# Kernel optimization log

Hardware: AMD Instinct MI355X
Metric: run time of the kernel (lower is better)

## Reference

```python
import jax, jax.numpy as jnp
import numpy as np

EMB = 1024

def setup_inputs() -> dict:
    key = jax.random.key(0)
    ks = jax.random.split(key, 6)
    T, k1, k2, D = 64, 256, 1024, EMB
    scale = 1.0 / np.sqrt(D)
    return {
        "fast_feature": jax.random.normal(ks[0], (T, k2, D), jnp.float32),
        "slow_feature": jax.random.normal(ks[1], (T, k1, D), jnp.float32),
        "fast_W": jax.random.normal(ks[2], (D, D), jnp.float32) * scale,
        "fast_b": jax.random.normal(ks[3], (D,), jnp.float32) * 0.01,
        "slow_W": jax.random.normal(ks[4], (D, D), jnp.float32) * scale,
        "slow_b": jax.random.normal(ks[5], (D,), jnp.float32) * 0.01,
    }

def reference(fast_feature, slow_feature, fast_W, fast_b, slow_W, slow_b):
    # Linear projections (torch Linear: x @ W.T + b)
    fast_key = jnp.einsum('tkd,ed->tke', fast_feature, fast_W) + fast_b  # [T,k2,D]
    slow_key = jnp.einsum('tkd,ed->tke', slow_feature, slow_W) + slow_b  # [T,k1,D]
    # Scaled dot-product similarity fast->slow
    sim = jnp.einsum('tqd,tkd->tqk', fast_key, slow_key)  # [T,k2,k1]
    sim = sim / jnp.sqrt(jnp.asarray(slow_feature.shape[-1], sim.dtype))
    attn = jax.nn.softmax(sim, axis=-1)
    ctx = jnp.einsum('tqk,tkd->tqd', attn, slow_feature)  # note: values are raw slow_feature
    return fast_feature + ctx
```

## Files before the change

kernel.cpp:

```cpp
#include <hip/hip_runtime.h>
#include <stdint.h>

typedef __attribute__((ext_vector_type(8))) short bf16x8;
typedef __attribute__((ext_vector_type(4))) float f32x4;

__device__ __forceinline__ unsigned short f2bf(float f) {
  unsigned int u = __builtin_bit_cast(unsigned int, f);
  u += 0x7FFFu + ((u >> 16) & 1u);
  return (unsigned short)(u >> 16);
}

__device__ __forceinline__ void gload_lds16(const void* g, void* l) {
  __builtin_amdgcn_global_load_lds(
      (__attribute__((address_space(1))) void*)(uintptr_t)g,
      (__attribute__((address_space(3))) void*)l,
      16, 0, 0);
}

#define BARRIER() do { asm volatile("" ::: "memory"); __builtin_amdgcn_s_barrier(); asm volatile("" ::: "memory"); } while (0)
#define WAITVM(N) asm volatile("s_waitcnt vmcnt(" #N ")" ::: "memory")

template <int MODE>
__global__ __launch_bounds__(512, 2) void gemm8(
    const unsigned short* __restrict__ A, const unsigned short* __restrict__ B,
    void* __restrict__ Cv, const float* __restrict__ aux, int N, int K,
    int nm, int nn, long sAB, long sBB, long sCB, long sXB, float scale)
{
  __shared__ __align__(16) char lds[131072];
  char* ldsc = lds;

  const int tid = threadIdx.x;
  const int lane = tid & 63;
  const int wid = tid >> 6;
  const int fr = lane & 15, fq = lane >> 4;

  const int nwg = gridDim.x;
  const int id = blockIdx.x;
  const int swz = (id & 7) * (nwg >> 3) + (id >> 3);
  const int per = nm * nn;
  const int t = swz / per;
  const int rem = swz - t * per;
  const int mi_ = rem / nn, ni_ = rem - mi_ * nn;
  const long bm = (long)mi_ * 256, bn = (long)ni_ * 256;

  const unsigned short* Ag = A + (long)t * sAB + bm * K;
  const unsigned short* Bg = B + (long)t * sBB + bn * K;
  const int NT = K >> 6;

  const unsigned short* aS[2][2];
  const unsigned short* bS[2][2];
#pragma unroll
  for (int p = 0; p < 2; ++p) {
    const int q = p * 512 + tid;
    const int lr = q >> 3, cs = q & 7;
    const int cl = cs ^ (lr & 7);
#pragma unroll
    for (int h = 0; h < 2; ++h) {
      const int gA = ((lr >> 6) << 7) | (h << 6) | (lr & 63);
      const int gB = ((lr >> 5) << 6) | (h << 5) | (lr & 31);
      aS[p][h] = Ag + (long)gA * K + cl * 8;
      bS[p][h] = Bg + (long)gB * K + cl * 8;
    }
  }

  const int c0 = ((fq ^ (fr & 3)) + ((fr >> 2) & 1) * 4) * 16;
  const int aRd = ((wid >> 2) * 64 + fr) * 128 + c0;
  const int bRd = ((wid & 3) * 32 + fr) * 128 + c0;

  f32x4 acc[2][2][4][2];
#pragma unroll
  for (int a = 0; a < 2; a++)
#pragma unroll
    for (int b = 0; b < 2; b++)
#pragma unroll
      for (int i = 0; i < 4; i++)
#pragma unroll
        for (int j = 0; j < 2; j++)
#pragma unroll
          for (int r = 0; r < 4; r++) acc[a][b][i][j][r] = 0.f;

  bf16x8 af[4][2], bf[2][2][2];

#define STAGE(srcArr, aoff, h, ktv, b) do {                                   \
  _Pragma("unroll")                                                           \
  for (int p = 0; p < 2; ++p)                                                 \
    gload_lds16(srcArr[p][h] + ((long)(ktv) << 6),                            \
                ldsc + (aoff) + ((b) << 16) + ((h) << 14) + (p << 13) + (wid << 10)); \
} while (0)

#define LDA(mi, cub) do {                                                     \
  _Pragma("unroll")                                                           \
  for (int i = 0; i < 4; ++i) {                                               \
    af[i][0] = *(const bf16x8*)(ldsc + (cub) + (mi) * 16384 + aRd + i * 2048);        \
    af[i][1] = *(const bf16x8*)(ldsc + (cub) + (mi) * 16384 + (aRd ^ 64) + i * 2048); \
  }                                                                           \
} while (0)

#define LDB(nj, cub) do {                                                     \
  _Pragma("unroll")                                                           \
  for (int j = 0; j < 2; ++j) {                                               \
    bf[nj][j][0] = *(const bf16x8*)(ldsc + 32768 + (cub) + (nj) * 16384 + bRd + j * 2048);        \
    bf[nj][j][1] = *(const bf16x8*)(ldsc + 32768 + (cub) + (nj) * 16384 + (bRd ^ 64) + j * 2048); \
  }                                                                           \
} while (0)

#define QUAD(mi, nj) do {                                                     \
  __builtin_amdgcn_s_setprio(1);                                              \
  _Pragma("unroll")                                                           \
  for (int i = 0; i < 4; ++i)                                                 \
  _Pragma("unroll")                                                           \
  for (int j = 0; j < 2; ++j) {                                               \
    acc[mi][nj][i][j] = __builtin_amdgcn_mfma_f32_16x16x32_bf16(              \
        af[i][0], bf[nj][j][0], acc[mi][nj][i][j], 0, 0, 0);                  \
    acc[mi][nj][i][j] = __builtin_amdgcn_mfma_f32_16x16x32_bf16(              \
        af[i][1], bf[nj][j][1], acc[mi][nj][i][j], 0, 0, 0);                  \
  }                                                                           \
  __builtin_amdgcn_s_setprio(0);                                              \
} while (0)

  STAGE(aS, 0, 0, 0, 0);
  STAGE(bS, 32768, 0, 0, 0);
  STAGE(bS, 32768, 1, 0, 0);
  STAGE(aS, 0, 1, 0, 0);
  if (NT > 1) {
    STAGE(aS, 0, 0, 1, 1);
    STAGE(bS, 32768, 0, 1, 1);
    STAGE(bS, 32768, 1, 1, 1);
    WAITVM(6);
  } else {
    WAITVM(0);
  }
  BARRIER();

  for (int kt = 0; kt < NT; ++kt) {
    const int cur = kt & 1, nxt = cur ^ 1;
    const int cub = cur << 16;
    LDA(0, cub);
    LDB(0, cub);
    if (kt + 1 < NT) STAGE(aS, 0, 1, kt + 1, nxt);
    BARRIER();
    QUAD(0, 0);
    BARRIER();
    LDB(1, cub);
    if (kt + 2 < NT) STAGE(aS, 0, 0, kt + 2, cur);
    BARRIER();
    QUAD(0, 1);
    BARRIER();
    LDA(1, cub);
    if (kt + 2 < NT) STAGE(bS, 32768, 0, kt + 2, cur);
    BARRIER();
    QUAD(1, 0);
    BARRIER();
    if (kt + 2 < NT) {
      STAGE(bS, 32768, 1, kt + 2, cur);
      QUAD(1, 1);
      WAITVM(6);
    } else {
      QUAD(1, 1);
      WAITVM(0);
    }
    BARRIER();
  }

  if (MODE == 1) {
    float* red  = (float*)ldsc;
    float* red2 = (float*)(ldsc + 4096);
    const int wc = wid & 3;
    const int rbase = (wid >> 2) * 128;
#pragma unroll
    for (int mi = 0; mi < 2; ++mi)
#pragma unroll
      for (int i = 0; i < 4; ++i)
#pragma unroll
        for (int r = 0; r < 4; ++r) {
          float m = fmaxf(fmaxf(acc[mi][0][i][0][r], acc[mi][0][i][1][r]),
                          fmaxf(acc[mi][1][i][0][r], acc[mi][1][i][1][r]));
#pragma unroll
          for (int o = 1; o <= 8; o <<= 1) m = fmaxf(m, __shfl_xor(m, o));
          if (fr == 0) red[(rbase + mi * 64 + i * 16 + fq * 4 + r) * 4 + wc] = m;
        }
    BARRIER();
#pragma unroll
    for (int mi = 0; mi < 2; ++mi)
#pragma unroll
      for (int i = 0; i < 4; ++i)
#pragma unroll
        for (int r = 0; r < 4; ++r) {
          const int rl = rbase + mi * 64 + i * 16 + fq * 4 + r;
          f32x4 mm = *(f32x4*)&red[rl * 4];
          const float M = fmaxf(fmaxf(mm[0], mm[1]), fmaxf(mm[2], mm[3]));
          float s = 0.f;
#pragma unroll
          for (int nj = 0; nj < 2; ++nj)
#pragma unroll
            for (int j = 0; j < 2; ++j) {
              float e = __expf((acc[mi][nj][i][j][r] - M) * scale);
              acc[mi][nj][i][j][r] = e;
              s += e;
            }
#pragma unroll
          for (int o = 1; o <= 8; o <<= 1) s += __shfl_xor(s, o);
          if (fr == 0) red2[rl * 4 + wc] = s;
        }
    BARRIER();
    unsigned short* C = (unsigned short*)Cv + (long)t * sCB;
#pragma unroll
    for (int mi = 0; mi < 2; ++mi)
#pragma unroll
      for (int i = 0; i < 4; ++i)
#pragma unroll
        for (int r = 0; r < 4; ++r) {
          const int rl = rbase + mi * 64 + i * 16 + fq * 4 + r;
          f32x4 sv = *(f32x4*)&red2[rl * 4];
          const float inv = 1.0f / (sv[0] + sv[1] + sv[2] + sv[3]);
          const long gr = bm + rl;
#pragma unroll
          for (int nj = 0; nj < 2; ++nj)
#pragma unroll
            for (int j = 0; j < 2; ++j) {
              const long gcol = bn + wc * 64 + nj * 32 + j * 16 + fr;
              C[gr * N + gcol] = f2bf(acc[mi][nj][i][j][r] * inv);
            }
        }
  } else {
#pragma unroll
    for (int mi = 0; mi < 2; ++mi)
#pragma unroll
      for (int nj = 0; nj < 2; ++nj)
#pragma unroll
        for (int i = 0; i < 4; ++i) {
          const long grow0 = bm + (wid >> 2) * 128 + mi * 64 + i * 16 + fq * 4;
#pragma unroll
          for (int j = 0; j < 2; ++j) {
            const long gcol = bn + (wid & 3) * 64 + nj * 32 + j * 16 + fr;
            if (MODE == 0) {
              unsigned short* C = (unsigned short*)Cv + (long)t * sCB;
              const float bv = aux[gcol];
#pragma unroll
              for (int r = 0; r < 4; ++r)
                C[(grow0 + r) * N + gcol] = f2bf(acc[mi][nj][i][j][r] + bv);
            } else {
              float* C = (float*)Cv + (long)t * sCB;
              const float* X = aux + (long)t * sXB;
#pragma unroll
              for (int r = 0; r < 4; ++r) {
                const long idx = (grow0 + r) * N + gcol;
                C[idx] = acc[mi][nj][i][j][r] + X[idx];
              }
            }
          }
        }
  }
#undef STAGE
#undef LDA
#undef LDB
#undef QUAD
}

__global__ __launch_bounds__(256) void convert_f32_bf16(
    const float* __restrict__ in, unsigned short* __restrict__ out, long n) {
  long i = ((long)blockIdx.x * 256 + threadIdx.x) * 4;
  long stride = (long)gridDim.x * 1024;
  for (; i < n; i += stride) {
    float4 v = *(const float4*)(in + i);
    ushort4 o;
    o.x = f2bf(v.x); o.y = f2bf(v.y); o.z = f2bf(v.z); o.w = f2bf(v.w);
    *(ushort4*)(out + i) = o;
  }
}

__global__ __launch_bounds__(256) void convert_transpose_slow(
    const float* __restrict__ in, unsigned short* __restrict__ outR,
    unsigned short* __restrict__ outT) {
  __shared__ unsigned short tile[32][33];
  int t = blockIdx.z;
  int d0 = blockIdx.x * 32;
  int k0 = blockIdx.y * 32;
  const float* ip = in + (long)t * 256 * 1024;
  unsigned short* rp = outR + (long)t * 256 * 1024;
  unsigned short* tp = outT + (long)t * 1024 * 256;
  int tx = threadIdx.x & 31, ty = threadIdx.x >> 5;
#pragma unroll
  for (int p = 0; p < 4; p++) {
    int k = ty + p * 8;
    unsigned short b = f2bf(ip[(long)(k0 + k) * 1024 + d0 + tx]);
    tile[k][tx] = b;
    rp[(long)(k0 + k) * 1024 + d0 + tx] = b;
  }
  __syncthreads();
#pragma unroll
  for (int p = 0; p < 4; p++) {
    int d = ty + p * 8;
    tp[(long)(d0 + d) * 256 + k0 + tx] = tile[tx][d];
  }
}

extern "C" void kernel_launch(void* const* d_in, const int* in_sizes, int n_in,
                              void* d_out, int out_size, void* d_ws, size_t ws_size,
                              hipStream_t stream) {
  const float* fastF     = (const float*)d_in[0];
  const float* slowF     = (const float*)d_in[1];
  const float* fastW     = (const float*)d_in[2];
  const float* fast_bias = (const float*)d_in[3];
  const float* slowW     = (const float*)d_in[4];
  const float* slow_bias = (const float*)d_in[5];
  float* out = (float*)d_out;

  char* ws = (char*)d_ws;
  unsigned short* fastBf  = (unsigned short*)(ws);
  unsigned short* attnBf  = (unsigned short*)(ws + 67108864L);
  unsigned short* fastKey = (unsigned short*)(ws + 134217728L);
  unsigned short* slowBf  = (unsigned short*)(ws + 268435456L);
  unsigned short* slowT   = (unsigned short*)(ws + 301989888L);
  unsigned short* slowKey = (unsigned short*)(ws + 335544320L);
  unsigned short* fWb     = (unsigned short*)(ws + 369098752L);
  unsigned short* sWb     = (unsigned short*)(ws + 371195904L);

  convert_f32_bf16<<<2048, 256, 0, stream>>>(fastF, fastBf, 67108864L);
  convert_f32_bf16<<<1024, 256, 0, stream>>>(fastW, fWb, 1048576L);
  convert_f32_bf16<<<1024, 256, 0, stream>>>(slowW, sWb, 1048576L);
  convert_transpose_slow<<<dim3(32, 8, 64), 256, 0, stream>>>(slowF, slowBf, slowT);

  gemm8<0><<<64 * 4, 512, 0, stream>>>(slowBf, sWb, slowKey, slow_bias,
      1024, 1024, 64, 4, 0, 0, 0, 0, 1.f);
  gemm8<0><<<256 * 4, 512, 0, stream>>>(fastBf, fWb, fastKey, fast_bias,
      1024, 1024, 256, 4, 0, 0, 0, 0, 1.f);
  gemm8<1><<<4 * 1 * 64, 512, 0, stream>>>(fastKey, slowKey, attnBf, nullptr,
      256, 1024, 4, 1, 1048576L, 262144L, 262144L, 0, 0.03125f);
  gemm8<2><<<4 * 4 * 64, 512, 0, stream>>>(attnBf, slowT, out, fastF,
      1024, 256, 4, 4, 262144L, 262144L, 1048576L, 1048576L, 1.f);
}
```

Before: 478.7 us.

## Make GEMM kernel persistent over multiple M tiles with continuous prefetch pipeline

Each workgroup now processes several consecutive 256-row M tiles (ntiles) in one flattened loop over tile×k steps. The global-to-LDS prefetch therefore runs across tile boundaries, and the epilogue runs inline before the accumulators are reset. All launches use 256 workgroups, which removes tail waves and pipeline ramp-up/drain per tile. The risks are epilogue stalls inside the loop and less parallelism for the fast-key GEMM and the final GEMM. The softmax epilogue also reuses LDS that may hold prefetched data for the next tile.

```diff
diff --git a/kernel.cpp b/kernel.cpp
--- a/kernel.cpp
+++ b/kernel.cpp
@@ -24,7 +24,8 @@
 __global__ __launch_bounds__(512, 2) void gemm8(
     const unsigned short* __restrict__ A, const unsigned short* __restrict__ B,
     void* __restrict__ Cv, const float* __restrict__ aux, int N, int K,
-    int nm, int nn, long sAB, long sBB, long sCB, long sXB, float scale)
+    int nm, int nn, int ntiles, long sAB, long sBB, long sCB, long sXB,
+    float scale)
 {
   __shared__ __align__(16) char lds[131072];
   char* ldsc = lds;
@@ -41,11 +42,16 @@
   const int t = swz / per;
   const int rem = swz - t * per;
   const int mi_ = rem / nn, ni_ = rem - mi_ * nn;
-  const long bm = (long)mi_ * 256, bn = (long)ni_ * 256;
-
-  const unsigned short* Ag = A + (long)t * sAB + bm * K;
+  const long bmBase = (long)mi_ * 256 * ntiles;
+  const long bn = (long)ni_ * 256;
+
+  const unsigned short* Ag = A + (long)t * sAB + bmBase * K;
   const unsigned short* Bg = B + (long)t * sBB + bn * K;
   const int NT = K >> 6;
+  const int lnt = __builtin_ctz(NT);
+  const int kmask = NT - 1;
+  const int G = ntiles << lnt;
+  const long tsA = (long)256 * K;
 
   const unsigned short* aS[2][2];
   const unsigned short* bS[2][2];
@@ -63,6 +69,9 @@
     }
   }
 
+#define AOFF(g) (((long)((g) & kmask) << 6) + (long)((g) >> lnt) * tsA)
+#define BOFF(g) ((long)((g) & kmask) << 6)
+
   const int c0 = ((fq ^ (fr & 3)) + ((fr >> 2) & 1) * 4) * 16;
   const int aRd = ((wid >> 2) * 64 + fr) * 128 + c0;
   const int bRd = ((wid & 3) * 32 + fr) * 128 + c0;
@@ -81,10 +90,10 @@
 
   bf16x8 af[4][2], bf[2][2][2];
 
-#define STAGE(srcArr, aoff, h, ktv, b) do {                                   \
+#define STAGE(srcArr, aoff, h, eoff, b) do {                                  \
   _Pragma("unroll")                                                           \
   for (int p = 0; p < 2; ++p)                                                 \
-    gload_lds16(srcArr[p][h] + ((long)(ktv) << 6),                            \
+    gload_lds16(srcArr[p][h] + (eoff),                                        \
                 ldsc + (aoff) + ((b) << 16) + ((h) << 14) + (p << 13) + (wid << 10)); \
 } while (0)
 
@@ -118,41 +127,41 @@
   __builtin_amdgcn_s_setprio(0);                                              \
 } while (0)
 
-  STAGE(aS, 0, 0, 0, 0);
-  STAGE(bS, 32768, 0, 0, 0);
-  STAGE(bS, 32768, 1, 0, 0);
-  STAGE(aS, 0, 1, 0, 0);
-  if (NT > 1) {
-    STAGE(aS, 0, 0, 1, 1);
-    STAGE(bS, 32768, 0, 1, 1);
-    STAGE(bS, 32768, 1, 1, 1);
+  STAGE(aS, 0, 0, AOFF(0), 0);
+  STAGE(bS, 32768, 0, BOFF(0), 0);
+  STAGE(bS, 32768, 1, BOFF(0), 0);
+  STAGE(aS, 0, 1, AOFF(0), 0);
+  if (G > 1) {
+    STAGE(aS, 0, 0, AOFF(1), 1);
+    STAGE(bS, 32768, 0, BOFF(1), 1);
+    STAGE(bS, 32768, 1, BOFF(1), 1);
     WAITVM(6);
   } else {
     WAITVM(0);
   }
   BARRIER();
 
-  for (int kt = 0; kt < NT; ++kt) {
-    const int cur = kt & 1, nxt = cur ^ 1;
+  for (int g = 0; g < G; ++g) {
+    const int cur = g & 1, nxt = cur ^ 1;
     const int cub = cur << 16;
     LDA(0, cub);
     LDB(0, cub);
-    if (kt + 1 < NT) STAGE(aS, 0, 1, kt + 1, nxt);
+    if (g + 1 < G) STAGE(aS, 0, 1, AOFF(g + 1), nxt);
     BARRIER();
     QUAD(0, 0);
     BARRIER();
     LDB(1, cub);
-    if (kt + 2 < NT) STAGE(aS, 0, 0, kt + 2, cur);
+    if (g + 2 < G) STAGE(aS, 0, 0, AOFF(g + 2), cur);
     BARRIER();
     QUAD(0, 1);
     BARRIER();
     LDA(1, cub);
-    if (kt + 2 < NT) STAGE(bS, 32768, 0, kt + 2, cur);
+    if (g + 2 < G) STAGE(bS, 32768, 0, BOFF(g + 2), cur);
     BARRIER();
     QUAD(1, 0);
     BARRIER();
-    if (kt + 2 < NT) {
-      STAGE(bS, 32768, 1, kt + 2, cur);
+    if (g + 2 < G) {
+      STAGE(bS, 32768, 1, BOFF(g + 2), cur);
       QUAD(1, 1);
       WAITVM(6);
     } else {
@@ -160,101 +169,117 @@
       WAITVM(0);
     }
     BARRIER();
-  }
-
-  if (MODE == 1) {
-    float* red  = (float*)ldsc;
-    float* red2 = (float*)(ldsc + 4096);
-    const int wc = wid & 3;
-    const int rbase = (wid >> 2) * 128;
-#pragma unroll
-    for (int mi = 0; mi < 2; ++mi)
-#pragma unroll
-      for (int i = 0; i < 4; ++i)
-#pragma unroll
-        for (int r = 0; r < 4; ++r) {
-          float m = fmaxf(fmaxf(acc[mi][0][i][0][r], acc[mi][0][i][1][r]),
-                          fmaxf(acc[mi][1][i][0][r], acc[mi][1][i][1][r]));
-#pragma unroll
-          for (int o = 1; o <= 8; o <<= 1) m = fmaxf(m, __shfl_xor(m, o));
-          if (fr == 0) red[(rbase + mi * 64 + i * 16 + fq * 4 + r) * 4 + wc] = m;
-        }
-    BARRIER();
-#pragma unroll
-    for (int mi = 0; mi < 2; ++mi)
-#pragma unroll
-      for (int i = 0; i < 4; ++i)
-#pragma unroll
-        for (int r = 0; r < 4; ++r) {
-          const int rl = rbase + mi * 64 + i * 16 + fq * 4 + r;
-          f32x4 mm = *(f32x4*)&red[rl * 4];
-          const float M = fmaxf(fmaxf(mm[0], mm[1]), fmaxf(mm[2], mm[3]));
-          float s = 0.f;
-#pragma unroll
-          for (int nj = 0; nj < 2; ++nj)
+
+    if ((g & kmask) != kmask) continue;
+
+    const int s = g >> lnt;
+    const long bm = bmBase + (long)s * 256;
+    if (MODE == 1) {
+      float* red  = (float*)ldsc;
+      float* red2 = (float*)(ldsc + 4096);
+      const int wc = wid & 3;
+      const int rbase = (wid >> 2) * 128;
+#pragma unroll
+      for (int mi = 0; mi < 2; ++mi)
+#pragma unroll
+        for (int i = 0; i < 4; ++i)
+#pragma unroll
+          for (int r = 0; r < 4; ++r) {
+            float m = fmaxf(fmaxf(acc[mi][0][i][0][r], acc[mi][0][i][1][r]),
+                            fmaxf(acc[mi][1][i][0][r], acc[mi][1][i][1][r]));
+#pragma unroll
+            for (int o = 1; o <= 8; o <<= 1) m = fmaxf(m, __shfl_xor(m, o));
+            if (fr == 0) red[(rbase + mi * 64 + i * 16 + fq * 4 + r) * 4 + wc] = m;
+          }
+      BARRIER();
+#pragma unroll
+      for (int mi = 0; mi < 2; ++mi)
+#pragma unroll
+        for (int i = 0; i < 4; ++i)
+#pragma unroll
+          for (int r = 0; r < 4; ++r) {
+            const int rl = rbase + mi * 64 + i * 16 + fq * 4 + r;
+            f32x4 mm = *(f32x4*)&red[rl * 4];
+            const float M = fmaxf(fmaxf(mm[0], mm[1]), fmaxf(mm[2], mm[3]));
+            float sm = 0.f;
+#pragma unroll
+            for (int nj = 0; nj < 2; ++nj)
+#pragma unroll
+              for (int j = 0; j < 2; ++j) {
+                float e = __expf((acc[mi][nj][i][j][r] - M) * scale);
+                acc[mi][nj][i][j][r] = e;
+                sm += e;
+              }
+#pragma unroll
+            for (int o = 1; o <= 8; o <<= 1) sm += __shfl_xor(sm, o);
+            if (fr == 0) red2[rl * 4 + wc] = sm;
+          }
+      BARRIER();
+      unsigned short* C = (unsigned short*)Cv + (long)t * sCB;
+#pragma unroll
+      for (int mi = 0; mi < 2; ++mi)
+#pragma unroll
+        for (int i = 0; i < 4; ++i)
+#pragma unroll
+          for (int r = 0; r < 4; ++r) {
+            const int rl = rbase + mi * 64 + i * 16 + fq * 4 + r;
+            f32x4 sv = *(f32x4*)&red2[rl * 4];
+            const float inv = 1.0f / (sv[0] + sv[1] + sv[2] + sv[3]);
+            const long gr = bm + rl;
+#pragma unroll
+            for (int nj = 0; nj < 2; ++nj)
+#pragma unroll
+              for (int j = 0; j < 2; ++j) {
+                const long gcol = bn + wc * 64 + nj * 32 + j * 16 + fr;
+                C[gr * N + gcol] = f2bf(acc[mi][nj][i][j][r] * inv);
+              }
+          }
+    } else {
+#pragma unroll
+      for (int mi = 0; mi < 2; ++mi)
+#pragma unroll
+        for (int nj = 0; nj < 2; ++nj)
+#pragma unroll
+          for (int i = 0; i < 4; ++i) {
+            const long grow0 = bm + (wid >> 2) * 128 + mi * 64 + i * 16 + fq * 4;
 #pragma unroll
             for (int j = 0; j < 2; ++j) {
-              float e = __expf((acc[mi][nj][i][j][r] - M) * scale);
-              acc[mi][nj][i][j][r] = e;
-              s += e;
-            }
-#pragma unroll
-          for (int o = 1; o <= 8; o <<= 1) s += __shfl_xor(s, o);
-          if (fr == 0) red2[rl * 4 + wc] = s;
-        }
-    BARRIER();
-    unsigned short* C = (unsigned short*)Cv + (long)t * sCB;
-#pragma unroll
-    for (int mi = 0; mi < 2; ++mi)
-#pragma unroll
-      for (int i = 0; i < 4; ++i)
-#pragma unroll
-        for (int r = 0; r < 4; ++r) {
-          const int rl = rbase + mi * 64 + i * 16 + fq * 4 + r;
-          f32x4 sv = *(f32x4*)&red2[rl * 4];
-          const float inv = 1.0f / (sv[0] + sv[1] + sv[2] + sv[3]);
-          const long gr = bm + rl;
-#pragma unroll
-          for (int nj = 0; nj < 2; ++nj)
-#pragma unroll
-            for (int j = 0; j < 2; ++j) {
-              const long gcol = bn + wc * 64 + nj * 32 + j * 16 + fr;
-              C[gr * N + gcol] = f2bf(acc[mi][nj][i][j][r] * inv);
-            }
-        }
-  } else {
-#pragma unroll
-    for (int mi = 0; mi < 2; ++mi)
-#pragma unroll
-      for (int nj = 0; nj < 2; ++nj)
-#pragma unroll
-        for (int i = 0; i < 4; ++i) {
-          const long grow0 = bm + (wid >> 2) * 128 + mi * 64 + i * 16 + fq * 4;
-#pragma unroll
-          for (int j = 0; j < 2; ++j) {
-            const long gcol = bn + (wid & 3) * 64 + nj * 32 + j * 16 + fr;
-            if (MODE == 0) {
-              unsigned short* C = (unsigned short*)Cv + (long)t * sCB;
-              const float bv = aux[gcol];
-#pragma unroll
-              for (int r = 0; r < 4; ++r)
-                C[(grow0 + r) * N + gcol] = f2bf(acc[mi][nj][i][j][r] + bv);
-            } else {
-              float* C = (float*)Cv + (long)t * sCB;
-              const float* X = aux + (long)t * sXB;
-#pragma unroll
-              for (int r = 0; r < 4; ++r) {
-                const long idx = (grow0 + r) * N + gcol;
-                C[idx] = acc[mi][nj][i][j][r] + X[idx];
+              const long gcol = bn + (wid & 3) * 64 + nj * 32 + j * 16 + fr;
+              if (MODE == 0) {
+                unsigned short* C = (unsigned short*)Cv + (long)t * sCB;
+                const float bv = aux[gcol];
+#pragma unroll
+                for (int r = 0; r < 4; ++r)
+                  C[(grow0 + r) * N + gcol] = f2bf(acc[mi][nj][i][j][r] + bv);
+              } else {
+                float* C = (float*)Cv + (long)t * sCB;
+                const float* X = aux + (long)t * sXB;
+#pragma unroll
+                for (int r = 0; r < 4; ++r) {
+                  const long idx = (grow0 + r) * N + gcol;
+                  C[idx] = acc[mi][nj][i][j][r] + X[idx];
+                }
               }
             }
           }
-        }
+#pragma unroll
+      for (int a = 0; a < 2; a++)
+#pragma unroll
+        for (int b = 0; b < 2; b++)
+#pragma unroll
+          for (int i = 0; i < 4; i++)
+#pragma unroll
+            for (int j = 0; j < 2; j++)
+#pragma unroll
+              for (int r = 0; r < 4; r++) acc[a][b][i][j][r] = 0.f;
+    }
   }
 #undef STAGE
 #undef LDA
 #undef LDB
 #undef QUAD
+#undef AOFF
+#undef BOFF
 }
 
 __global__ __launch_bounds__(256) void convert_f32_bf16(
@@ -321,12 +346,12 @@
   convert_f32_bf16<<<1024, 256, 0, stream>>>(slowW, sWb, 1048576L);
   convert_transpose_slow<<<dim3(32, 8, 64), 256, 0, stream>>>(slowF, slowBf, slowT);
 
-  gemm8<0><<<64 * 4, 512, 0, stream>>>(slowBf, sWb, slowKey, slow_bias,
-      1024, 1024, 64, 4, 0, 0, 0, 0, 1.f);
-  gemm8<0><<<256 * 4, 512, 0, stream>>>(fastBf, fWb, fastKey, fast_bias,
-      1024, 1024, 256, 4, 0, 0, 0, 0, 1.f);
-  gemm8<1><<<4 * 1 * 64, 512, 0, stream>>>(fastKey, slowKey, attnBf, nullptr,
-      256, 1024, 4, 1, 1048576L, 262144L, 262144L, 0, 0.03125f);
-  gemm8<2><<<4 * 4 * 64, 512, 0, stream>>>(attnBf, slowT, out, fastF,
-      1024, 256, 4, 4, 262144L, 262144L, 1048576L, 1048576L, 1.f);
-}
+  gemm8<0><<<256, 512, 0, stream>>>(slowBf, sWb, slowKey, slow_bias,
+      1024, 1024, 64, 4, 1, 0, 0, 0, 0, 1.f);
+  gemm8<0><<<256, 512, 0, stream>>>(fastBf, fWb, fastKey, fast_bias,
+      1024, 1024, 64, 4, 4, 0, 0, 0, 0, 1.f);
+  gemm8<1><<<256, 512, 0, stream>>>(fastKey, slowKey, attnBf, nullptr,
+      256, 1024, 4, 1, 1, 1048576L, 262144L, 262144L, 0, 0.03125f);
+  gemm8<2><<<256, 512, 0, stream>>>(attnBf, slowT, out, fastF,
+      1024, 256, 1, 4, 4, 262144L, 262144L, 1048576L, 1048576L, 1.f);
+}
```

Result: slower. 552.4 us (+15.4%).
